# Kernel optimization log

Measured on AMD Instinct MI355X. Metric: run time of the kernel, lower is better.

The kernel has to match this reference:

```python
import jax, jax.numpy as jnp
import numpy as np

D = 256; NH = 8; NL = 4; NP = 4; HD = D // NH
SHAPES = np.array([[180, 180], [90, 90], [45, 45], [23, 23]], dtype=np.int32)
LQ = int((SHAPES[:, 0] * SHAPES[:, 1]).sum())  # 43054
STARTS = np.concatenate([[0], np.cumsum(SHAPES[:, 0] * SHAPES[:, 1])[:-1]]).astype(np.int32)


def setup_inputs():
    ks = jax.random.split(jax.random.key(0), 16)
    s = 0.02
    p = lambda k, shp: jax.random.normal(k, shp, jnp.float32) * s
    return {
        "query": jax.random.normal(ks[0], (1, LQ, D), jnp.float32),
        "ref_points": jax.random.uniform(ks[1], (1, LQ, NL, 2), dtype=jnp.float32),
        "pos": jax.random.normal(ks[2], (1, LQ, D), jnp.float32),
        "input_spatial_shapes": jnp.asarray(SHAPES),
        "input_level_start_index": jnp.asarray(STARTS),
        "w_off": p(ks[3], (D, NH * NL * NP * 2)), "b_off": p(ks[4], (NH * NL * NP * 2,)),
        "w_attn": p(ks[5], (D, NH * NL * NP)), "b_attn": p(ks[6], (NH * NL * NP,)),
        "w_val": p(ks[7], (D, D)), "b_val": jnp.zeros((D,), jnp.float32),
        "w_out": p(ks[8], (D, D)), "b_out": jnp.zeros((D,), jnp.float32),
        "g1": jnp.ones((D,), jnp.float32), "beta1": jnp.zeros((D,), jnp.float32),
        "w1": p(ks[9], (D, D)), "b1": jnp.zeros((D,), jnp.float32),
        "w2": p(ks[10], (D, D)), "b2": jnp.zeros((D,), jnp.float32),
        "g2": jnp.ones((D,), jnp.float32), "beta2": jnp.zeros((D,), jnp.float32),
    }


def _ln(x, g, b):
    m = x.mean(-1, keepdims=True)
    v = ((x - m) ** 2).mean(-1, keepdims=True)
    return (x - m) * jax.lax.rsqrt(v + 1e-5) * g + b


def _sample_level(v, Hl, Wl, loc):
    # v: (B, Hl*Wl, NH, HD); loc: (B, Lq, NH, NP, 2) normalized to [0,1]
    # Bilinear sampling matching F.grid_sample(align_corners=False, padding_mode='zeros')
    B, _, nh, d = v.shape
    Lq, P = loc.shape[1], loc.shape[3]
    vb = jnp.transpose(v, (0, 2, 1, 3))  # (B, NH, HW, d)
    x = loc[..., 0] * Wl - 0.5
    y = loc[..., 1] * Hl - 0.5
    x0 = jnp.floor(x); y0 = jnp.floor(y)
    fx = x - x0; fy = y - y0
    out = jnp.zeros((B, nh, Lq, P, d), v.dtype)
    for dy in (0, 1):
        for dx in (0, 1):
            xi = x0 + dx; yi = y0 + dy
            w = (fx if dx else 1.0 - fx) * (fy if dy else 1.0 - fy)
            valid = (xi >= 0) & (xi < Wl) & (yi >= 0) & (yi < Hl)
            xc = jnp.clip(xi, 0, Wl - 1).astype(jnp.int32)
            yc = jnp.clip(yi, 0, Hl - 1).astype(jnp.int32)
            idx = jnp.transpose(yc * Wl + xc, (0, 2, 1, 3)).reshape(B, nh, Lq * P)
            g = jnp.take_along_axis(vb, idx[..., None], axis=2).reshape(B, nh, Lq, P, d)
            wt = jnp.transpose(jnp.where(valid, w, 0.0), (0, 2, 1, 3))
            out = out + g * wt[..., None]
    return out  # (B, NH, Lq, NP, HD)


def _layer(query, ref_points, pos, shp, sti, w_off, b_off, w_attn, b_attn, w_val, b_val,
           w_out, b_out, g1, beta1, w1, b1, w2, b2, g2, beta2):
    B, Lq, _ = query.shape
    q = query + pos  # with_pos_embed
    value = (query @ w_val + b_val).reshape(B, Lq, NH, HD)
    off = (q @ w_off + b_off).reshape(B, Lq, NH, NL, NP, 2)
    aw = jax.nn.softmax((q @ w_attn + b_attn).reshape(B, Lq, NH, NL * NP), axis=-1)
    aw = aw.reshape(B, Lq, NH, NL, NP)
    # offset_normalizer = [W_l, H_l]
    norm = jnp.asarray(shp[:, ::-1].copy(), jnp.float32)
    loc = ref_points[:, :, None, :, None, :] + off / norm[None, None, None, :, None, :]
    acc = jnp.zeros((B, NH, Lq, HD), query.dtype)
    for l in range(NL):
        Hl, Wl = int(shp[l, 0]), int(shp[l, 1])
        st = int(sti[l])
        sampled = _sample_level(value[:, st:st + Hl * Wl], Hl, Wl, loc[:, :, :, l])
        wl = jnp.transpose(aw[:, :, :, l], (0, 2, 1, 3))  # (B, NH, Lq, NP)
        acc = acc + (sampled * wl[..., None]).sum(axis=3)
    attn_out = acc.transpose(0, 2, 1, 3).reshape(B, Lq, D) @ w_out + b_out
    # residual + LayerNorm + FFN (dropout is identity in eval mode)
    x = _ln(query + attn_out, g1, beta1)
    ffn = jax.nn.relu(x @ w1 + b1) @ w2 + b2
    return _ln(x + ffn, g2, beta2)


def reference(query, ref_points, pos, input_spatial_shapes, input_level_start_index,
              w_off, b_off, w_attn, b_attn, w_val, b_val, w_out, b_out,
              g1, beta1, w1, b1, w2, b2, g2, beta2):
    shp = np.asarray(input_spatial_shapes)
    sti = np.asarray(input_level_start_index)
    return _layer(query, ref_points, pos, shp, sti, w_off, b_off, w_attn, b_attn,
                  w_val, b_val, w_out, b_out, g1, beta1, w1, b1, w2, b2, g2, beta2)
```

## Files before the change

kernel.cpp:

```cpp
#include <hip/hip_runtime.h>

typedef unsigned short u16;
typedef unsigned int u32;
typedef float f32x4 __attribute__((ext_vector_type(4)));
typedef short i16x8 __attribute__((ext_vector_type(8)));
typedef __bf16 bf16x8_t __attribute__((ext_vector_type(8)));

#define LQ 43054

__device__ __forceinline__ float bf2f(u16 u) {
  union { u32 i; float f; } v; v.i = ((u32)u) << 16; return v.f;
}
__device__ __forceinline__ u16 f2bf(float f) {
  u32 i = __float_as_uint(f);
  return (u16)((i + 0x7FFFu + ((i >> 16) & 1u)) >> 16);
}

__device__ __forceinline__ float dot2bf(u32 v, u32 w, float c) {
  float d;
  asm("v_dot2_f32_bf16 %0, %1, %2, %3" : "=v"(d) : "v"(v), "v"(w), "v"(c));
  return d;
}

template <typename T>
__device__ __forceinline__ auto mfma_try(T a, T b, f32x4 c, int)
    -> decltype(__builtin_amdgcn_mfma_f32_16x16x32_bf16(a, b, c, 0, 0, 0)) {
  return __builtin_amdgcn_mfma_f32_16x16x32_bf16(a, b, c, 0, 0, 0);
}
template <typename T>
__device__ __forceinline__ f32x4 mfma_try(T a, T b, f32x4 c, long) {
  return __builtin_amdgcn_mfma_f32_16x16x32_bf16(
      __builtin_bit_cast(bf16x8_t, a), __builtin_bit_cast(bf16x8_t, b), c, 0, 0, 0);
}
__device__ __forceinline__ f32x4 mfma_bf16(i16x8 a, i16x8 b, f32x4 c) {
  return mfma_try(a, b, c, 0);
}

__global__ void transpose_all_kernel(
    const float* __restrict__ w_off, const float* __restrict__ w_attn,
    const float* __restrict__ w_val, const float* __restrict__ w_out,
    const float* __restrict__ w1, const float* __restrict__ w2,
    u16* __restrict__ wT) {
  int b = blockIdx.x;
  const float* src; u16* dst; int N; int col;
  if (b < 256)       { src = w_off;  dst = wT;          N = 256; col = b; }
  else if (b < 384)  { src = w_attn; dst = wT + 65536;  N = 128; col = b - 256; }
  else if (b < 640)  { src = w_val;  dst = wT + 98304;  N = 256; col = b - 384; }
  else if (b < 896)  { src = w_out;  dst = wT + 163840; N = 256; col = b - 640; }
  else if (b < 1152) { src = w1;     dst = wT + 229376; N = 256; col = b - 896; }
  else               { src = w2;     dst = wT + 294912; N = 256; col = b - 1152; }
  dst[col * 256 + threadIdx.x] = f2bf(src[threadIdx.x * N + col]);
}

__device__ __forceinline__ void stage_a_dma(uint4* As, const u16* A, int r0, int M,
                                            int w, int lane) {
#pragma unroll
  for (int jj = 0; jj < 8; ++jj) {
    int row = w * 16 + jj * 2 + (lane >> 5);
    int gr = min(r0 + row, M - 1);
    int c = lane & 31;
    const uint4* gp = (const uint4*)A + (size_t)gr * 32 + (c ^ (row & 7));
    __builtin_amdgcn_global_load_lds(
        (const __attribute__((address_space(1))) void*)gp,
        (__attribute__((address_space(3))) void*)(As + (w * 16 + jj * 2) * 32),
        16, 0, 0);
  }
}
template <int ADD, int PH>
__device__ __forceinline__ void stage_a_f32(uint4* As, const float* A, const float* A2,
                                            int r0, int M, int tid) {
  constexpr int IT = 16 / PH;
#pragma unroll
  for (int h = 0; h < PH; ++h) {
    float4 va[IT];
    float4 vp[ADD ? IT : 1];
#pragma unroll
    for (int it = 0; it < IT; ++it) {
      int e = tid + (h * IT + it) * 256;
      int gr = min(r0 + (e >> 6), M - 1);
      int idx = gr * 64 + (e & 63);
      va[it] = ((const float4*)A)[idx];
      if constexpr (ADD) vp[it] = ((const float4*)A2)[idx];
    }
#pragma unroll
    for (int it = 0; it < IT; ++it) {
      int e = tid + (h * IT + it) * 256;
      int row = e >> 6, c4 = e & 63;
      float4 v = va[it];
      if constexpr (ADD) {
        v.x += vp[it].x; v.y += vp[it].y; v.z += vp[it].z; v.w += vp[it].w;
      }
      uint2 pk;
      pk.x = (u32)f2bf(v.x) | ((u32)f2bf(v.y) << 16);
      pk.y = (u32)f2bf(v.z) | ((u32)f2bf(v.w) << 16);
      int c = c4 >> 1, hf = c4 & 1;
      ((uint2*)As)[((row * 32 + (c ^ (row & 7))) << 1) | hf] = pk;
    }
  }
}
__device__ __forceinline__ void load_b(i16x8* f, const u16* Bt, int t, int l16, int quad) {
  const uint4* bp = (const uint4*)Bt + (t * 16 + l16) * 32 + quad;
#pragma unroll
  for (int kk = 0; kk < 8; ++kk) f[kk] = __builtin_bit_cast(i16x8, bp[kk << 2]);
}
__device__ __forceinline__ void tile_mfma(f32x4* acc, const uint4* As,
                                          const i16x8* bfr, int l16, int quad) {
#pragma unroll
  for (int rg = 0; rg < 4; ++rg) {
    int arow = rg * 16 + l16;
    f32x4 a = {0.f, 0.f, 0.f, 0.f};
#pragma unroll
    for (int kk = 0; kk < 8; ++kk) {
      i16x8 afr = __builtin_bit_cast(i16x8, As[arow * 32 + (((kk << 2) + quad) ^ (arow & 7))]);
      a = mfma_bf16(afr, bfr[kk], a);
    }
    acc[rg] = a;
  }
}
__device__ __forceinline__ void tile_mfma2(f32x4* acc, const uint4* As,
                                           const i16x8* bfr, int l16, int quad) {
#pragma unroll
  for (int rg = 0; rg < 2; ++rg) {
    int arow = rg * 16 + l16;
    f32x4 a = {0.f, 0.f, 0.f, 0.f};
#pragma unroll
    for (int kk = 0; kk < 8; ++kk) {
      i16x8 afr = __builtin_bit_cast(i16x8, As[arow * 32 + (((kk << 2) + quad) ^ (arow & 7))]);
      a = mfma_bf16(afr, bfr[kk], a);
    }
    acc[rg] = a;
  }
}

__device__ __forceinline__ int swz_u16(int row, int col) {
  return row * 256 + ((((col >> 3) ^ (row & 7)) << 3) | (col & 7));
}

#define LS_STRIDE 264
__device__ __forceinline__ void lds_store_rows(const u16* Ls, u16* out,
                                               int r0, int M, int w, int lane) {
#pragma unroll
  for (int it = 0; it < 8; ++it) {
    int lrow = w * 16 + it * 2 + (lane >> 5);
    int grow = r0 + lrow;
    int chunk = lane & 31;
    if (grow < M) {
      *(uint4*)(out + (size_t)grow * 256 + chunk * 8) =
          *(const uint4*)(Ls + lrow * LS_STRIDE + chunk * 8);
    }
  }
}

template <int AIN, int MODE>
__global__ __launch_bounds__(256, 3) void gemm_kernel(
    const void* __restrict__ Av, const u16* __restrict__ Bt,
    const float* __restrict__ bias, void* __restrict__ out, int M) {
  __shared__ uint4 As[2176];
  const int tid = threadIdx.x;
  const int w = tid >> 6, lane = tid & 63, quad = lane >> 4, l16 = lane & 15;
  const int r0 = blockIdx.x * 64;
  if constexpr (AIN == 2) stage_a_dma(As, (const u16*)Av, r0, M, w, lane);
  else                    stage_a_f32<0, 2>(As, (const float*)Av, nullptr, r0, M, tid);
  __syncthreads();
  i16x8 bfr[2][8];
  load_b(bfr[0], Bt, w * 4, l16, quad);
  f32x4 vals[4][4];
#pragma unroll
  for (int i = 0; i < 4; ++i) {
    const int t = w * 4 + i;
    if (i + 1 < 4) load_b(bfr[(i + 1) & 1], Bt, t + 1, l16, quad);
    tile_mfma(vals[i], As, bfr[i & 1], l16, quad);
  }
  __syncthreads();
  u16* Ls = (u16*)As;
#pragma unroll
  for (int i = 0; i < 4; ++i) {
    const int col = (w * 4 + i) * 16 + l16;
    const float bv = bias[col];
#pragma unroll
    for (int rg = 0; rg < 4; ++rg)
#pragma unroll
      for (int r = 0; r < 4; ++r) {
        float v = vals[i][rg][r] + bv;
        if (MODE == 2) v = fmaxf(v, 0.f);
        Ls[(rg * 16 + (quad << 2) + r) * LS_STRIDE + col] = f2bf(v);
      }
  }
  __syncthreads();
  lds_store_rows(Ls, (u16*)out, r0, M, w, lane);
}

__global__ __launch_bounds__(256, 3) void offaw_gemm_kernel(
    const float* __restrict__ query, const float* __restrict__ pos,
    const u16* __restrict__ Bt, const float* __restrict__ b_off,
    const float* __restrict__ b_attn, u16* __restrict__ offb,
    float* __restrict__ aw, int M) {
  __shared__ uint4 As[2176];
  const int tid = threadIdx.x;
  const int w = tid >> 6, lane = tid & 63, quad = lane >> 4, l16 = lane & 15;
  const int r0 = blockIdx.x * 64;
  stage_a_f32<1, 4>(As, query, pos, r0, M, tid);
  __syncthreads();
  i16x8 bfr[2][8];
  load_b(bfr[0], Bt, w, l16, quad);
  f32x4 vals[4][4];
#pragma unroll
  for (int i = 0; i < 6; ++i) {
    const int t = w + 4 * i;
    if (i + 1 < 6) load_b(bfr[(i + 1) & 1], Bt, w + 4 * (i + 1), l16, quad);
    if (i < 4) {
      tile_mfma(vals[i], As, bfr[i & 1], l16, quad);
    } else {
      f32x4 acc[4];
      tile_mfma(acc, As, bfr[i & 1], l16, quad);
      const int colc = (t - 16) * 16 + l16;
      const float bv = b_attn[colc];
#pragma unroll
      for (int rg = 0; rg < 4; ++rg)
#pragma unroll
        for (int r = 0; r < 4; ++r) {
          float v = acc[rg][r] + bv;
          float m = v;
#pragma unroll
          for (int o = 1; o < 16; o <<= 1) m = fmaxf(m, __shfl_xor(m, o));
          float e = __expf(v - m);
          float s = e;
#pragma unroll
          for (int o = 1; o < 16; o <<= 1) s += __shfl_xor(s, o);
          int row = r0 + rg * 16 + (quad << 2) + r;
          if (row < M) aw[row * 128 + colc] = e / s;
        }
    }
  }
  __syncthreads();
  u16* Ls = (u16*)As;
#pragma unroll
  for (int i = 0; i < 4; ++i) {
    const int col = (w + 4 * i) * 16 + l16;
    const float bv = b_off[col];
#pragma unroll
    for (int rg = 0; rg < 4; ++rg)
#pragma unroll
      for (int r = 0; r < 4; ++r)
        Ls[(rg * 16 + (quad << 2) + r) * LS_STRIDE + col] = f2bf(vals[i][rg][r] + bv);
  }
  __syncthreads();
  lds_store_rows(Ls, offb, r0, M, w, lane);
}

__global__ __launch_bounds__(256, 4) void tail_fused_kernel(
    const u16* __restrict__ accb, const u16* __restrict__ woutT,
    const float* __restrict__ b_out, const float* __restrict__ query,
    const float* __restrict__ g1, const float* __restrict__ beta1,
    const u16* __restrict__ w1T, const float* __restrict__ b1,
    const u16* __restrict__ w2T, const float* __restrict__ b2,
    const float* __restrict__ g2, const float* __restrict__ beta2,
    float* __restrict__ out, int M) {
  __shared__ uint4 smem[2112];
  uint4* As = smem;
  uint4* Xs = smem + 1024;
  float2* pnorm = (float2*)(smem + 2048);
  const int tid = threadIdx.x;
  const int w = tid >> 6, lane = tid & 63, quad = lane >> 4, l16 = lane & 15;
  const int r0 = blockIdx.x * 32;
#pragma unroll
  for (int jj = 0; jj < 4; ++jj) {
    int row = w * 8 + jj * 2 + (lane >> 5);
    int gr = min(r0 + row, M - 1);
    int c = lane & 31;
    const uint4* gp = (const uint4*)accb + (size_t)gr * 32 + (c ^ (row & 7));
    __builtin_amdgcn_global_load_lds(
        (const __attribute__((address_space(1))) void*)gp,
        (__attribute__((address_space(3))) void*)(As + (w * 8 + jj * 2) * 32),
        16, 0, 0);
  }
  __syncthreads();
  i16x8 bfr[8];
  f32x4 vals[4][2];
  float s[8], s2[8];

#pragma unroll
  for (int i = 0; i < 4; ++i) {
    load_b(bfr, woutT, w * 4 + i, l16, quad);
    tile_mfma2(vals[i], As, bfr, l16, quad);
  }
#pragma unroll
  for (int k = 0; k < 8; ++k) { s[k] = 0.f; s2[k] = 0.f; }
#pragma unroll
  for (int i = 0; i < 4; ++i) {
    const int col = (w * 4 + i) * 16 + l16;
    const float bv = b_out[col];
#pragma unroll
    for (int rg = 0; rg < 2; ++rg)
#pragma unroll
      for (int r = 0; r < 4; ++r) {
        int row = r0 + rg * 16 + (quad << 2) + r;
        float rv = (row < M) ? query[row * 256 + col] : 0.f;
        float v = vals[i][rg][r] + bv + rv;
        vals[i][rg][r] = v;
        s[rg * 4 + r] += v; s2[rg * 4 + r] += v * v;
      }
  }
#pragma unroll
  for (int k = 0; k < 8; ++k)
#pragma unroll
    for (int o = 1; o < 16; o <<= 1) {
      s[k] += __shfl_xor(s[k], o);
      s2[k] += __shfl_xor(s2[k], o);
    }
  if (l16 == 0) {
#pragma unroll
    for (int rg = 0; rg < 2; ++rg)
#pragma unroll
      for (int r = 0; r < 4; ++r)
        pnorm[(rg * 16 + (quad << 2) + r) * 4 + w] = make_float2(s[rg * 4 + r], s2[rg * 4 + r]);
  }
  __syncthreads();
  u16* Xu = (u16*)Xs;
#pragma unroll
  for (int rg = 0; rg < 2; ++rg)
#pragma unroll
    for (int r = 0; r < 4; ++r) {
      int lrow = rg * 16 + (quad << 2) + r;
      float4 p01 = ((const float4*)pnorm)[lrow * 2];
      float4 p23 = ((const float4*)pnorm)[lrow * 2 + 1];
      float ss = p01.x + p01.z + p23.x + p23.z;
      float qq = p01.y + p01.w + p23.y + p23.w;
      float mean = ss * (1.f / 256.f);
      float var = qq * (1.f / 256.f) - mean * mean;
      float inv = rsqrtf(var + 1e-5f);
#pragma unroll
      for (int i = 0; i < 4; ++i) {
        const int col = (w * 4 + i) * 16 + l16;
        float o = (vals[i][rg][r] - mean) * inv * g1[col] + beta1[col];
        Xu[swz_u16(lrow, col)] = f2bf(o);
      }
    }
  __syncthreads();

#pragma unroll
  for (int i = 0; i < 4; ++i) {
    load_b(bfr, w1T, w * 4 + i, l16, quad);
    tile_mfma2(vals[i], Xs, bfr, l16, quad);
  }
  u16* Hu = (u16*)As;
#pragma unroll
  for (int i = 0; i < 4; ++i) {
    const int col = (w * 4 + i) * 16 + l16;
    const float bv = b1[col];
#pragma unroll
    for (int rg = 0; rg < 2; ++rg)
#pragma unroll
      for (int r = 0; r < 4; ++r) {
        int lrow = rg * 16 + (quad << 2) + r;
        Hu[swz_u16(lrow, col)] = f2bf(fmaxf(vals[i][rg][r] + bv, 0.f));
      }
  }
  __syncthreads();

#pragma unroll
  for (int i = 0; i < 4; ++i) {
    load_b(bfr, w2T, w * 4 + i, l16, quad);
    tile_mfma2(vals[i], As, bfr, l16, quad);
  }
#pragma unroll
  for (int k = 0; k < 8; ++k) { s[k] = 0.f; s2[k] = 0.f; }
#pragma unroll
  for (int i = 0; i < 4; ++i) {
    const int col = (w * 4 + i) * 16 + l16;
    const float bv = b2[col];
#pragma unroll
    for (int rg = 0; rg < 2; ++rg)
#pragma unroll
      for (int r = 0; r < 4; ++r) {
        int lrow = rg * 16 + (quad << 2) + r;
        float xv = bf2f(Xu[swz_u16(lrow, col)]);
        float v = vals[i][rg][r] + bv + xv;
        vals[i][rg][r] = v;
        s[rg * 4 + r] += v; s2[rg * 4 + r] += v * v;
      }
  }
#pragma unroll
  for (int k = 0; k < 8; ++k)
#pragma unroll
    for (int o = 1; o < 16; o <<= 1) {
      s[k] += __shfl_xor(s[k], o);
      s2[k] += __shfl_xor(s2[k], o);
    }
  if (l16 == 0) {
#pragma unroll
    for (int rg = 0; rg < 2; ++rg)
#pragma unroll
      for (int r = 0; r < 4; ++r)
        pnorm[(rg * 16 + (quad << 2) + r) * 4 + w] = make_float2(s[rg * 4 + r], s2[rg * 4 + r]);
  }
  __syncthreads();
  float* stg = (float*)smem;
#pragma unroll
  for (int rg = 0; rg < 2; ++rg) {
#pragma unroll
    for (int r = 0; r < 4; ++r) {
      int lrow = rg * 16 + (quad << 2) + r;
      float4 p01 = ((const float4*)pnorm)[lrow * 2];
      float4 p23 = ((const float4*)pnorm)[lrow * 2 + 1];
      float ss = p01.x + p01.z + p23.x + p23.z;
      float qq = p01.y + p01.w + p23.y + p23.w;
      float mean = ss * (1.f / 256.f);
      float var = qq * (1.f / 256.f) - mean * mean;
      float inv = rsqrtf(var + 1e-5f);
#pragma unroll
      for (int i = 0; i < 4; ++i) {
        const int col = (w * 4 + i) * 16 + l16;
        stg[((quad << 2) + r) * 268 + col] = (vals[i][rg][r] - mean) * inv * g2[col] + beta2[col];
      }
    }
    __syncthreads();
#pragma unroll
    for (int rr = 0; rr < 4; ++rr) {
      int lr = w * 4 + rr;
      int grow = r0 + rg * 16 + lr;
      if (grow < M)
        *(float4*)(out + (size_t)grow * 256 + lane * 4) =
            *(const float4*)(stg + lr * 268 + lane * 4);
    }
    if (rg == 0) __syncthreads();
  }
}

__global__ __launch_bounds__(256) void sampler_kernel(
    const float* __restrict__ refp, const u16* __restrict__ offb,
    const float* __restrict__ aw, const u16* __restrict__ value,
    u32* __restrict__ accv) {
  __shared__ uint4 rec[544];
  const int t = threadIdx.x;
  const int nwg = gridDim.x;
  const int qd = nwg >> 3, rm = nwg & 7;
  const int xcd = blockIdx.x & 7, ii = blockIdx.x >> 3;
  const int b = (xcd < rm ? xcd * (qd + 1) : rm * (qd + 1) + (xcd - rm) * qd) + ii;
#pragma unroll
  for (int it = 0; it < 2; ++it) {
    const int sidx = t + it * 256;
    const int qs = sidx >> 7, j = sidx & 127;
    const int i = b * 4 + qs;
    if (i < LQ) {
      const int h = j >> 4, lp = j & 15, l = lp >> 2;
      const int Wl = (l == 0) ? 180 : (l == 1) ? 90 : (l == 2) ? 45 : 23;
      const int st = (l == 0) ? 0 : (l == 1) ? 32400 : (l == 2) ? 40500 : 42525;
      const float wj = aw[i * 128 + j];
      const u32 o2 = *(const u32*)(offb + i * 256 + h * 32 + lp * 2);
      const float ox = bf2f((u16)(o2 & 0xffffu)), oy = bf2f((u16)(o2 >> 16));
      const float rx = refp[i * 8 + l * 2], ry = refp[i * 8 + l * 2 + 1];
      float x = rx * (float)Wl + ox - 0.5f;
      float y = ry * (float)Wl + oy - 0.5f;
      float x0f = floorf(x), y0f = floorf(y);
      float fx = x - x0f, fy = y - y0f;
      int x0 = (int)x0f, y0 = (int)y0f;
      bool vx0 = (x0 >= 0) & (x0 < Wl), vx1 = (x0 + 1 >= 0) & (x0 + 1 < Wl);
      bool vy0 = (y0 >= 0) & (y0 < Wl), vy1 = (y0 + 1 >= 0) & (y0 + 1 < Wl);
      int x0c = min(max(x0, 0), Wl - 1), x1c = min(max(x0 + 1, 0), Wl - 1);
      int y0c = min(max(y0, 0), Wl - 1), y1c = min(max(y0 + 1, 0), Wl - 1);
      float w00 = (vx0 & vy0) ? wj * (1.f - fx) * (1.f - fy) : 0.f;
      float w01 = (vx1 & vy0) ? wj * fx * (1.f - fy) : 0.f;
      float w10 = (vx0 & vy1) ? wj * (1.f - fx) * fy : 0.f;
      float w11 = (vx1 & vy1) ? wj * fx * fy : 0.f;
      uint4 r;
      r.x = (u32)((st + y0c * Wl + x0c) * 512 + h * 64) | (u32)(x1c - x0c);
      r.y = (u32)(y1c - y0c) * (u32)(Wl * 512);
      r.z = (u32)f2bf(w00) | ((u32)f2bf(w01) << 16);
      r.w = (u32)f2bf(w10) | ((u32)f2bf(w11) << 16);
      rec[qs * 136 + h * 17 + lp] = r;
    }
  }
  __syncthreads();
  const int qs = t >> 6, j2 = t & 63;
  const int h = j2 >> 3, dp8 = j2 & 7;
  const int i = b * 4 + qs;
  if (i >= LQ) return;
  const char* vb = (const char*)value;
  float a0 = 0.f, a1 = 0.f, a2 = 0.f, a3 = 0.f;
  const int rbase = qs * 136 + h * 17;
  const u32 dpo = (u32)(dp8 * 8);
#pragma unroll
  for (int p = 0; p < 16; ++p) {
    uint4 r = rec[rbase + p];
    u32 base = (r.x & 0xFFFFFFFEu) + dpo;
    u32 dxo = (r.x & 1u) << 9;
    u32 dyo = r.y;
    uint2 p00 = *(const uint2*)(vb + base);
    uint2 p01 = *(const uint2*)(vb + base + dxo);
    uint2 p10 = *(const uint2*)(vb + base + dyo);
    uint2 p11 = *(const uint2*)(vb + base + dyo + dxo);
    a0 = dot2bf(__builtin_amdgcn_perm(p01.x, p00.x, 0x05040100u), r.z, a0);
    a1 = dot2bf(__builtin_amdgcn_perm(p01.x, p00.x, 0x07060302u), r.z, a1);
    a2 = dot2bf(__builtin_amdgcn_perm(p01.y, p00.y, 0x05040100u), r.z, a2);
    a3 = dot2bf(__builtin_amdgcn_perm(p01.y, p00.y, 0x07060302u), r.z, a3);
    a0 = dot2bf(__builtin_amdgcn_perm(p11.x, p10.x, 0x05040100u), r.w, a0);
    a1 = dot2bf(__builtin_amdgcn_perm(p11.x, p10.x, 0x07060302u), r.w, a1);
    a2 = dot2bf(__builtin_amdgcn_perm(p11.y, p10.y, 0x05040100u), r.w, a2);
    a3 = dot2bf(__builtin_amdgcn_perm(p11.y, p10.y, 0x07060302u), r.w, a3);
  }
  uint2 pk;
  pk.x = (u32)f2bf(a0) | ((u32)f2bf(a1) << 16);
  pk.y = (u32)f2bf(a2) | ((u32)f2bf(a3) << 16);
  ((uint2*)accv)[i * 64 + h * 8 + dp8] = pk;
}

extern "C" void kernel_launch(void* const* d_in, const int* in_sizes, int n_in,
                              void* d_out, int out_size, void* d_ws, size_t ws_size,
                              hipStream_t stream) {
  const float* query  = (const float*)d_in[0];
  const float* refp   = (const float*)d_in[1];
  const float* pos    = (const float*)d_in[2];
  const float* w_off  = (const float*)d_in[5];
  const float* b_off  = (const float*)d_in[6];
  const float* w_attn = (const float*)d_in[7];
  const float* b_attn = (const float*)d_in[8];
  const float* w_val  = (const float*)d_in[9];
  const float* b_val  = (const float*)d_in[10];
  const float* w_out  = (const float*)d_in[11];
  const float* b_out  = (const float*)d_in[12];
  const float* g1     = (const float*)d_in[13];
  const float* beta1  = (const float*)d_in[14];
  const float* w1     = (const float*)d_in[15];
  const float* b1     = (const float*)d_in[16];
  const float* w2     = (const float*)d_in[17];
  const float* b2     = (const float*)d_in[18];
  const float* g2     = (const float*)d_in[19];
  const float* beta2  = (const float*)d_in[20];

  char* ws = (char*)d_ws;
  u16*   wT    = (u16*)(ws + 0);
  u16*   value = (u16*)(ws + 720896);
  u16*   offb  = (u16*)(ws + 22764544);
  float* aw    = (float*)(ws + 44808192);
  u16*   accb  = (u16*)(ws + 66851840);

  u16* woffT  = wT;
  u16* wvalT  = wT + 98304;
  u16* woutT  = wT + 163840;
  u16* w1T    = wT + 229376;
  u16* w2T    = wT + 294912;

  transpose_all_kernel<<<1408, 256, 0, stream>>>(w_off, w_attn, w_val, w_out, w1, w2, wT);

  const int gm = (LQ + 63) / 64;
  gemm_kernel<0, 1><<<gm, 256, 0, stream>>>(query, wvalT, b_val, value, LQ);
  offaw_gemm_kernel<<<gm, 256, 0, stream>>>(query, pos, woffT, b_off, b_attn, offb, aw, LQ);
  const int sb = (LQ + 3) / 4;
  sampler_kernel<<<sb, 256, 0, stream>>>(refp, offb, aw, value, (u32*)accb);
  const int gt = (LQ + 31) / 32;
  tail_fused_kernel<<<gt, 256, 0, stream>>>(accb, woutT, b_out, query, g1, beta1,
                                            w1T, b1, w2T, b2, g2, beta2,
                                            (float*)d_out, LQ);
}
```

Measured before the change: 394.4 us.

## Fuse value and offset/attention GEMMs into one kernel; shrink sampler blocks

Merges the value-projection GEMM and the offset/attention-weight GEMM into a single kernel over 32-row tiles. Query and query+pos are read once and staged together in LDS, which removes one kernel launch and a second read of query. The sampler now handles 2 queries per block with 4-byte gathers per thread instead of 4 queries with 8-byte gathers, and the XCD-aware block remapping is dropped. The trade-off is more, smaller blocks, less memory-level parallelism per thread in the sampler, and the loss of L2 locality from the XCD remap.

```diff
diff --git a/kernel.cpp b/kernel.cpp
--- a/kernel.cpp
+++ b/kernel.cpp
@@ -52,61 +52,15 @@
   dst[col * 256 + threadIdx.x] = f2bf(src[threadIdx.x * N + col]);
 }
 
-__device__ __forceinline__ void stage_a_dma(uint4* As, const u16* A, int r0, int M,
-                                            int w, int lane) {
-#pragma unroll
-  for (int jj = 0; jj < 8; ++jj) {
-    int row = w * 16 + jj * 2 + (lane >> 5);
-    int gr = min(r0 + row, M - 1);
-    int c = lane & 31;
-    const uint4* gp = (const uint4*)A + (size_t)gr * 32 + (c ^ (row & 7));
-    __builtin_amdgcn_global_load_lds(
-        (const __attribute__((address_space(1))) void*)gp,
-        (__attribute__((address_space(3))) void*)(As + (w * 16 + jj * 2) * 32),
-        16, 0, 0);
-  }
-}
-template <int ADD, int PH>
-__device__ __forceinline__ void stage_a_f32(uint4* As, const float* A, const float* A2,
-                                            int r0, int M, int tid) {
-  constexpr int IT = 16 / PH;
-#pragma unroll
-  for (int h = 0; h < PH; ++h) {
-    float4 va[IT];
-    float4 vp[ADD ? IT : 1];
-#pragma unroll
-    for (int it = 0; it < IT; ++it) {
-      int e = tid + (h * IT + it) * 256;
-      int gr = min(r0 + (e >> 6), M - 1);
-      int idx = gr * 64 + (e & 63);
-      va[it] = ((const float4*)A)[idx];
-      if constexpr (ADD) vp[it] = ((const float4*)A2)[idx];
-    }
-#pragma unroll
-    for (int it = 0; it < IT; ++it) {
-      int e = tid + (h * IT + it) * 256;
-      int row = e >> 6, c4 = e & 63;
-      float4 v = va[it];
-      if constexpr (ADD) {
-        v.x += vp[it].x; v.y += vp[it].y; v.z += vp[it].z; v.w += vp[it].w;
-      }
-      uint2 pk;
-      pk.x = (u32)f2bf(v.x) | ((u32)f2bf(v.y) << 16);
-      pk.y = (u32)f2bf(v.z) | ((u32)f2bf(v.w) << 16);
-      int c = c4 >> 1, hf = c4 & 1;
-      ((uint2*)As)[((row * 32 + (c ^ (row & 7))) << 1) | hf] = pk;
-    }
-  }
-}
 __device__ __forceinline__ void load_b(i16x8* f, const u16* Bt, int t, int l16, int quad) {
   const uint4* bp = (const uint4*)Bt + (t * 16 + l16) * 32 + quad;
 #pragma unroll
   for (int kk = 0; kk < 8; ++kk) f[kk] = __builtin_bit_cast(i16x8, bp[kk << 2]);
 }
-__device__ __forceinline__ void tile_mfma(f32x4* acc, const uint4* As,
-                                          const i16x8* bfr, int l16, int quad) {
-#pragma unroll
-  for (int rg = 0; rg < 4; ++rg) {
+__device__ __forceinline__ void tile_mfma2(f32x4* acc, const uint4* As,
+                                           const i16x8* bfr, int l16, int quad) {
+#pragma unroll
+  for (int rg = 0; rg < 2; ++rg) {
     int arow = rg * 16 + l16;
     f32x4 a = {0.f, 0.f, 0.f, 0.f};
 #pragma unroll
@@ -117,135 +71,132 @@
     acc[rg] = a;
   }
 }
-__device__ __forceinline__ void tile_mfma2(f32x4* acc, const uint4* As,
-                                           const i16x8* bfr, int l16, int quad) {
-#pragma unroll
-  for (int rg = 0; rg < 2; ++rg) {
-    int arow = rg * 16 + l16;
-    f32x4 a = {0.f, 0.f, 0.f, 0.f};
-#pragma unroll
-    for (int kk = 0; kk < 8; ++kk) {
-      i16x8 afr = __builtin_bit_cast(i16x8, As[arow * 32 + (((kk << 2) + quad) ^ (arow & 7))]);
-      a = mfma_bf16(afr, bfr[kk], a);
-    }
-    acc[rg] = a;
-  }
-}
 
 __device__ __forceinline__ int swz_u16(int row, int col) {
   return row * 256 + ((((col >> 3) ^ (row & 7)) << 3) | (col & 7));
 }
 
 #define LS_STRIDE 264
-__device__ __forceinline__ void lds_store_rows(const u16* Ls, u16* out,
-                                               int r0, int M, int w, int lane) {
-#pragma unroll
-  for (int it = 0; it < 8; ++it) {
-    int lrow = w * 16 + it * 2 + (lane >> 5);
-    int grow = r0 + lrow;
-    int chunk = lane & 31;
-    if (grow < M) {
-      *(uint4*)(out + (size_t)grow * 256 + chunk * 8) =
-          *(const uint4*)(Ls + lrow * LS_STRIDE + chunk * 8);
-    }
-  }
-}
-
-template <int AIN, int MODE>
-__global__ __launch_bounds__(256, 3) void gemm_kernel(
-    const void* __restrict__ Av, const u16* __restrict__ Bt,
-    const float* __restrict__ bias, void* __restrict__ out, int M) {
-  __shared__ uint4 As[2176];
+
+__global__ __launch_bounds__(256, 4) void valoff_kernel(
+    const float* __restrict__ query, const float* __restrict__ pos,
+    const u16* __restrict__ wvalT, const float* __restrict__ b_val,
+    const u16* __restrict__ woffT, const float* __restrict__ b_off,
+    const float* __restrict__ b_attn,
+    u16* __restrict__ value, u16* __restrict__ offb, float* __restrict__ aw,
+    int M) {
+  __shared__ uint4 smem[2112];
+  uint4* Aq  = smem;
+  uint4* Aqp = smem + 1088;
   const int tid = threadIdx.x;
   const int w = tid >> 6, lane = tid & 63, quad = lane >> 4, l16 = lane & 15;
-  const int r0 = blockIdx.x * 64;
-  if constexpr (AIN == 2) stage_a_dma(As, (const u16*)Av, r0, M, w, lane);
-  else                    stage_a_f32<0, 2>(As, (const float*)Av, nullptr, r0, M, tid);
-  __syncthreads();
-  i16x8 bfr[2][8];
-  load_b(bfr[0], Bt, w * 4, l16, quad);
-  f32x4 vals[4][4];
-#pragma unroll
-  for (int i = 0; i < 4; ++i) {
-    const int t = w * 4 + i;
-    if (i + 1 < 4) load_b(bfr[(i + 1) & 1], Bt, t + 1, l16, quad);
-    tile_mfma(vals[i], As, bfr[i & 1], l16, quad);
-  }
-  __syncthreads();
-  u16* Ls = (u16*)As;
+  const int r0 = blockIdx.x * 32;
+#pragma unroll
+  for (int h = 0; h < 2; ++h) {
+    float4 vq[4], vp[4];
+#pragma unroll
+    for (int it = 0; it < 4; ++it) {
+      int e = tid + (h * 4 + it) * 256;
+      int gr = min(r0 + (e >> 6), M - 1);
+      int idx = gr * 64 + (e & 63);
+      vq[it] = ((const float4*)query)[idx];
+      vp[it] = ((const float4*)pos)[idx];
+    }
+#pragma unroll
+    for (int it = 0; it < 4; ++it) {
+      int e = tid + (h * 4 + it) * 256;
+      int row = e >> 6, c4 = e & 63;
+      int c = c4 >> 1, hf = c4 & 1;
+      int sidx = ((row * 32 + (c ^ (row & 7))) << 1) | hf;
+      uint2 pkq, pks;
+      pkq.x = (u32)f2bf(vq[it].x) | ((u32)f2bf(vq[it].y) << 16);
+      pkq.y = (u32)f2bf(vq[it].z) | ((u32)f2bf(vq[it].w) << 16);
+      float sx = vq[it].x + vp[it].x, sy = vq[it].y + vp[it].y;
+      float sz = vq[it].z + vp[it].z, sw = vq[it].w + vp[it].w;
+      pks.x = (u32)f2bf(sx) | ((u32)f2bf(sy) << 16);
+      pks.y = (u32)f2bf(sz) | ((u32)f2bf(sw) << 16);
+      ((uint2*)Aq)[sidx] = pkq;
+      ((uint2*)Aqp)[sidx] = pks;
+    }
+  }
+  __syncthreads();
+  i16x8 bfr[8];
+  f32x4 vals[4][2];
+#pragma unroll
+  for (int i = 0; i < 4; ++i) {
+    load_b(bfr, wvalT, w * 4 + i, l16, quad);
+    tile_mfma2(vals[i], Aq, bfr, l16, quad);
+  }
+#pragma unroll
+  for (int i = 0; i < 2; ++i) {
+    const int t = w + 4 * i;
+    f32x4 acc[2];
+    load_b(bfr, woffT, 16 + t, l16, quad);
+    tile_mfma2(acc, Aqp, bfr, l16, quad);
+    const int colc = t * 16 + l16;
+    const float bv = b_attn[colc];
+#pragma unroll
+    for (int rg = 0; rg < 2; ++rg)
+#pragma unroll
+      for (int r = 0; r < 4; ++r) {
+        float v = acc[rg][r] + bv;
+        float m = v;
+#pragma unroll
+        for (int o = 1; o < 16; o <<= 1) m = fmaxf(m, __shfl_xor(m, o));
+        float e = __expf(v - m);
+        float s = e;
+#pragma unroll
+        for (int o = 1; o < 16; o <<= 1) s += __shfl_xor(s, o);
+        int row = r0 + rg * 16 + (quad << 2) + r;
+        if (row < M) aw[row * 128 + colc] = e / s;
+      }
+  }
+  __syncthreads();
+  u16* Ls = (u16*)smem;
 #pragma unroll
   for (int i = 0; i < 4; ++i) {
     const int col = (w * 4 + i) * 16 + l16;
-    const float bv = bias[col];
-#pragma unroll
-    for (int rg = 0; rg < 4; ++rg)
-#pragma unroll
-      for (int r = 0; r < 4; ++r) {
-        float v = vals[i][rg][r] + bv;
-        if (MODE == 2) v = fmaxf(v, 0.f);
-        Ls[(rg * 16 + (quad << 2) + r) * LS_STRIDE + col] = f2bf(v);
-      }
-  }
-  __syncthreads();
-  lds_store_rows(Ls, (u16*)out, r0, M, w, lane);
-}
-
-__global__ __launch_bounds__(256, 3) void offaw_gemm_kernel(
-    const float* __restrict__ query, const float* __restrict__ pos,
-    const u16* __restrict__ Bt, const float* __restrict__ b_off,
-    const float* __restrict__ b_attn, u16* __restrict__ offb,
-    float* __restrict__ aw, int M) {
-  __shared__ uint4 As[2176];
-  const int tid = threadIdx.x;
-  const int w = tid >> 6, lane = tid & 63, quad = lane >> 4, l16 = lane & 15;
-  const int r0 = blockIdx.x * 64;
-  stage_a_f32<1, 4>(As, query, pos, r0, M, tid);
-  __syncthreads();
-  i16x8 bfr[2][8];
-  load_b(bfr[0], Bt, w, l16, quad);
-  f32x4 vals[4][4];
-#pragma unroll
-  for (int i = 0; i < 6; ++i) {
-    const int t = w + 4 * i;
-    if (i + 1 < 6) load_b(bfr[(i + 1) & 1], Bt, w + 4 * (i + 1), l16, quad);
-    if (i < 4) {
-      tile_mfma(vals[i], As, bfr[i & 1], l16, quad);
-    } else {
-      f32x4 acc[4];
-      tile_mfma(acc, As, bfr[i & 1], l16, quad);
-      const int colc = (t - 16) * 16 + l16;
-      const float bv = b_attn[colc];
-#pragma unroll
-      for (int rg = 0; rg < 4; ++rg)
-#pragma unroll
-        for (int r = 0; r < 4; ++r) {
-          float v = acc[rg][r] + bv;
-          float m = v;
-#pragma unroll
-          for (int o = 1; o < 16; o <<= 1) m = fmaxf(m, __shfl_xor(m, o));
-          float e = __expf(v - m);
-          float s = e;
-#pragma unroll
-          for (int o = 1; o < 16; o <<= 1) s += __shfl_xor(s, o);
-          int row = r0 + rg * 16 + (quad << 2) + r;
-          if (row < M) aw[row * 128 + colc] = e / s;
-        }
-    }
-  }
-  __syncthreads();
-  u16* Ls = (u16*)As;
-#pragma unroll
-  for (int i = 0; i < 4; ++i) {
-    const int col = (w + 4 * i) * 16 + l16;
-    const float bv = b_off[col];
-#pragma unroll
-    for (int rg = 0; rg < 4; ++rg)
+    const float bv = b_val[col];
+#pragma unroll
+    for (int rg = 0; rg < 2; ++rg)
 #pragma unroll
       for (int r = 0; r < 4; ++r)
         Ls[(rg * 16 + (quad << 2) + r) * LS_STRIDE + col] = f2bf(vals[i][rg][r] + bv);
   }
   __syncthreads();
-  lds_store_rows(Ls, offb, r0, M, w, lane);
+#pragma unroll
+  for (int it = 0; it < 4; ++it) {
+    int lrow = w * 8 + it * 2 + (lane >> 5);
+    int grow = r0 + lrow;
+    if (grow < M)
+      *(uint4*)(value + (size_t)grow * 256 + (lane & 31) * 8) =
+          *(const uint4*)(Ls + lrow * LS_STRIDE + (lane & 31) * 8);
+  }
+#pragma unroll
+  for (int i = 0; i < 4; ++i) {
+    load_b(bfr, woffT, w * 4 + i, l16, quad);
+    tile_mfma2(vals[i], Aqp, bfr, l16, quad);
+  }
+  __syncthreads();
+#pragma unroll
+  for (int i = 0; i < 4; ++i) {
+    const int col = (w * 4 + i) * 16 + l16;
+    const float bv = b_off[col];
+#pragma unroll
+    for (int rg = 0; rg < 2; ++rg)
+#pragma unroll
+      for (int r = 0; r < 4; ++r)
+        Ls[(rg * 16 + (quad << 2) + r) * LS_STRIDE + col] = f2bf(vals[i][rg][r] + bv);
+  }
+  __syncthreads();
+#pragma unroll
+  for (int it = 0; it < 4; ++it) {
+    int lrow = w * 8 + it * 2 + (lane >> 5);
+    int grow = r0 + lrow;
+    if (grow < M)
+      *(uint4*)(offb + (size_t)grow * 256 + (lane & 31) * 8) =
+          *(const uint4*)(Ls + lrow * LS_STRIDE + (lane & 31) * 8);
+  }
 }
 
 __global__ __launch_bounds__(256, 4) void tail_fused_kernel(
@@ -431,78 +382,63 @@
     const float* __restrict__ refp, const u16* __restrict__ offb,
     const float* __restrict__ aw, const u16* __restrict__ value,
     u32* __restrict__ accv) {
-  __shared__ uint4 rec[544];
+  __shared__ uint4 rec[272];
   const int t = threadIdx.x;
-  const int nwg = gridDim.x;
-  const int qd = nwg >> 3, rm = nwg & 7;
-  const int xcd = blockIdx.x & 7, ii = blockIdx.x >> 3;
-  const int b = (xcd < rm ? xcd * (qd + 1) : rm * (qd + 1) + (xcd - rm) * qd) + ii;
-#pragma unroll
-  for (int it = 0; it < 2; ++it) {
-    const int sidx = t + it * 256;
-    const int qs = sidx >> 7, j = sidx & 127;
-    const int i = b * 4 + qs;
-    if (i < LQ) {
-      const int h = j >> 4, lp = j & 15, l = lp >> 2;
-      const int Wl = (l == 0) ? 180 : (l == 1) ? 90 : (l == 2) ? 45 : 23;
-      const int st = (l == 0) ? 0 : (l == 1) ? 32400 : (l == 2) ? 40500 : 42525;
-      const float wj = aw[i * 128 + j];
-      const u32 o2 = *(const u32*)(offb + i * 256 + h * 32 + lp * 2);
-      const float ox = bf2f((u16)(o2 & 0xffffu)), oy = bf2f((u16)(o2 >> 16));
-      const float rx = refp[i * 8 + l * 2], ry = refp[i * 8 + l * 2 + 1];
-      float x = rx * (float)Wl + ox - 0.5f;
-      float y = ry * (float)Wl + oy - 0.5f;
-      float x0f = floorf(x), y0f = floorf(y);
-      float fx = x - x0f, fy = y - y0f;
-      int x0 = (int)x0f, y0 = (int)y0f;
-      bool vx0 = (x0 >= 0) & (x0 < Wl), vx1 = (x0 + 1 >= 0) & (x0 + 1 < Wl);
-      bool vy0 = (y0 >= 0) & (y0 < Wl), vy1 = (y0 + 1 >= 0) & (y0 + 1 < Wl);
-      int x0c = min(max(x0, 0), Wl - 1), x1c = min(max(x0 + 1, 0), Wl - 1);
-      int y0c = min(max(y0, 0), Wl - 1), y1c = min(max(y0 + 1, 0), Wl - 1);
-      float w00 = (vx0 & vy0) ? wj * (1.f - fx) * (1.f - fy) : 0.f;
-      float w01 = (vx1 & vy0) ? wj * fx * (1.f - fy) : 0.f;
-      float w10 = (vx0 & vy1) ? wj * (1.f - fx) * fy : 0.f;
-      float w11 = (vx1 & vy1) ? wj * fx * fy : 0.f;
-      uint4 r;
-      r.x = (u32)((st + y0c * Wl + x0c) * 512 + h * 64) | (u32)(x1c - x0c);
-      r.y = (u32)(y1c - y0c) * (u32)(Wl * 512);
-      r.z = (u32)f2bf(w00) | ((u32)f2bf(w01) << 16);
-      r.w = (u32)f2bf(w10) | ((u32)f2bf(w11) << 16);
-      rec[qs * 136 + h * 17 + lp] = r;
-    }
-  }
-  __syncthreads();
-  const int qs = t >> 6, j2 = t & 63;
-  const int h = j2 >> 3, dp8 = j2 & 7;
-  const int i = b * 4 + qs;
-  if (i >= LQ) return;
+  const int b = blockIdx.x;
+  {
+    const int qs = t >> 7, j = t & 127;
+    const int i = b * 2 + qs;
+    const int h = j >> 4, lp = j & 15, l = lp >> 2;
+    const int Wl = (l == 0) ? 180 : (l == 1) ? 90 : (l == 2) ? 45 : 23;
+    const int st = (l == 0) ? 0 : (l == 1) ? 32400 : (l == 2) ? 40500 : 42525;
+    const float wj = aw[i * 128 + j];
+    const u32 o2 = *(const u32*)(offb + i * 256 + h * 32 + lp * 2);
+    const float ox = bf2f((u16)(o2 & 0xffffu)), oy = bf2f((u16)(o2 >> 16));
+    const float rx = refp[i * 8 + l * 2], ry = refp[i * 8 + l * 2 + 1];
+    float x = rx * (float)Wl + ox - 0.5f;
+    float y = ry * (float)Wl + oy - 0.5f;
+    float x0f = floorf(x), y0f = floorf(y);
+    float fx = x - x0f, fy = y - y0f;
+    int x0 = (int)x0f, y0 = (int)y0f;
+    bool vx0 = (x0 >= 0) & (x0 < Wl), vx1 = (x0 + 1 >= 0) & (x0 + 1 < Wl);
+    bool vy0 = (y0 >= 0) & (y0 < Wl), vy1 = (y0 + 1 >= 0) & (y0 + 1 < Wl);
+    int x0c = min(max(x0, 0), Wl - 1), x1c = min(max(x0 + 1, 0), Wl - 1);
+    int y0c = min(max(y0, 0), Wl - 1), y1c = min(max(y0 + 1, 0), Wl - 1);
+    float w00 = (vx0 & vy0) ? wj * (1.f - fx) * (1.f - fy) : 0.f;
+    float w01 = (vx1 & vy0) ? wj * fx * (1.f - fy) : 0.f;
+    float w10 = (vx0 & vy1) ? wj * (1.f - fx) * fy : 0.f;
+    float w11 = (vx1 & vy1) ? wj * fx * fy : 0.f;
+    uint4 r;
+    r.x = (u32)((st + y0c * Wl + x0c) * 512 + h * 64) | (u32)(x1c - x0c);
+    r.y = (u32)(y1c - y0c) * (u32)(Wl * 512);
+    r.z = (u32)f2bf(w00) | ((u32)f2bf(w01) << 16);
+    r.w = (u32)f2bf(w10) | ((u32)f2bf(w11) << 16);
+    rec[qs * 136 + h * 17 + lp] = r;
+  }
+  __syncthreads();
+  const int qs = t >> 7, j = t & 127;
+  const int h = j >> 4, dp = j & 15;
   const char* vb = (const char*)value;
-  float a0 = 0.f, a1 = 0.f, a2 = 0.f, a3 = 0.f;
+  float a0 = 0.f, a1 = 0.f;
   const int rbase = qs * 136 + h * 17;
-  const u32 dpo = (u32)(dp8 * 8);
+  const u32 dp4 = (u32)(dp * 4);
 #pragma unroll
   for (int p = 0; p < 16; ++p) {
     uint4 r = rec[rbase + p];
-    u32 base = (r.x & 0xFFFFFFFEu) + dpo;
+    u32 base = (r.x & 0xFFFFFFFEu) + dp4;
     u32 dxo = (r.x & 1u) << 9;
     u32 dyo = r.y;
-    uint2 p00 = *(const uint2*)(vb + base);
-    uint2 p01 = *(const uint2*)(vb + base + dxo);
-    uint2 p10 = *(const uint2*)(vb + base + dyo);
-    uint2 p11 = *(const uint2*)(vb + base + dyo + dxo);
-    a0 = dot2bf(__builtin_amdgcn_perm(p01.x, p00.x, 0x05040100u), r.z, a0);
-    a1 = dot2bf(__builtin_amdgcn_perm(p01.x, p00.x, 0x07060302u), r.z, a1);
-    a2 = dot2bf(__builtin_amdgcn_perm(p01.y, p00.y, 0x05040100u), r.z, a2);
-    a3 = dot2bf(__builtin_amdgcn_perm(p01.y, p00.y, 0x07060302u), r.z, a3);
-    a0 = dot2bf(__builtin_amdgcn_perm(p11.x, p10.x, 0x05040100u), r.w, a0);
-    a1 = dot2bf(__builtin_amdgcn_perm(p11.x, p10.x, 0x07060302u), r.w, a1);
-    a2 = dot2bf(__builtin_amdgcn_perm(p11.y, p10.y, 0x05040100u), r.w, a2);
-    a3 = dot2bf(__builtin_amdgcn_perm(p11.y, p10.y, 0x07060302u), r.w, a3);
-  }
-  uint2 pk;
-  pk.x = (u32)f2bf(a0) | ((u32)f2bf(a1) << 16);
-  pk.y = (u32)f2bf(a2) | ((u32)f2bf(a3) << 16);
-  ((uint2*)accv)[i * 64 + h * 8 + dp8] = pk;
+    u32 p00 = *(const u32*)(vb + base);
+    u32 p01 = *(const u32*)(vb + base + dxo);
+    u32 p10 = *(const u32*)(vb + base + dyo);
+    u32 p11 = *(const u32*)(vb + base + dyo + dxo);
+    a0 = dot2bf(__builtin_amdgcn_perm(p01, p00, 0x05040100u), r.z, a0);
+    a1 = dot2bf(__builtin_amdgcn_perm(p01, p00, 0x07060302u), r.z, a1);
+    a0 = dot2bf(__builtin_amdgcn_perm(p11, p10, 0x05040100u), r.w, a0);
+    a1 = dot2bf(__builtin_amdgcn_perm(p11, p10, 0x07060302u), r.w, a1);
+  }
+  u32 pk = (u32)f2bf(a0) | ((u32)f2bf(a1) << 16);
+  accv[(b * 2 + qs) * 128 + j] = pk;
 }
 
 extern "C" void kernel_launch(void* const* d_in, const int* in_sizes, int n_in,
@@ -543,13 +479,11 @@
 
   transpose_all_kernel<<<1408, 256, 0, stream>>>(w_off, w_attn, w_val, w_out, w1, w2, wT);
 
-  const int gm = (LQ + 63) / 64;
-  gemm_kernel<0, 1><<<gm, 256, 0, stream>>>(query, wvalT, b_val, value, LQ);
-  offaw_gemm_kernel<<<gm, 256, 0, stream>>>(query, pos, woffT, b_off, b_attn, offb, aw, LQ);
-  const int sb = (LQ + 3) / 4;
-  sampler_kernel<<<sb, 256, 0, stream>>>(refp, offb, aw, value, (u32*)accb);
-  const int gt = (LQ + 31) / 32;
-  tail_fused_kernel<<<gt, 256, 0, stream>>>(accb, woutT, b_out, query, g1, beta1,
+  const int gh = (LQ + 31) / 32;
+  valoff_kernel<<<gh, 256, 0, stream>>>(query, pos, wvalT, b_val, woffT, b_off, b_attn,
+                                        value, offb, aw, LQ);
+  sampler_kernel<<<LQ / 2, 256, 0, stream>>>(refp, offb, aw, value, (u32*)accb);
+  tail_fused_kernel<<<gh, 256, 0, stream>>>(accb, woutT, b_out, query, g1, beta1,
                                             w1T, b1, w2T, b2, g2, beta2,
                                             (float*)d_out, LQ);
 }
```

After: 393.4 us. Within noise of the previous version (-0.3%).
